# Kernel tuning notes

Measured on AMD Instinct MI355X. Metric: run time of the kernel, lower is better.

## Reference

```python
import jax, jax.numpy as jnp
import numpy as np


def setup_inputs() -> dict:
    key = jax.random.key(0)
    ks = jax.random.split(key, 7)
    T, B, D, H, Q = 256, 128, 1024, 2048, 1024
    return {
        "x": jax.random.normal(ks[0], (T, B, D), dtype=jnp.float32),
        "h0": jax.random.normal(ks[1], (B, H), dtype=jnp.float32) * 0.01,
        "W_xh": jax.random.normal(ks[2], (D, H), dtype=jnp.float32) * 0.01,
        "W_hh": jax.random.normal(ks[3], (H, H), dtype=jnp.float32) * 0.01,
        "b_h": jnp.zeros((H,), dtype=jnp.float32),
        "W_hq": jax.random.normal(ks[4], (H, Q), dtype=jnp.float32) * 0.01,
        "b_q": jnp.zeros((Q,), dtype=jnp.float32),
    }


def reference(x, h0, W_xh, W_hh, b_h, W_hq, b_q):
    # x: (T, B, D); vanilla RNN recurrence with ReLU, per-step output projection.
    def step(h, xt):
        h = jax.nn.relu(xt @ W_xh + h @ W_hh + b_h)  # (B, H)
        return h, h @ W_hq + b_q                      # (B, Q)

    h, outs = jax.lax.scan(step, h0, x)               # outs: (T, B, Q)
    out = outs.reshape(-1, outs.shape[-1])            # torch.cat along dim 0 -> (T*B, Q)
    return out, h
```

## Files before the change

kernel.cpp:

```cpp
#include <hip/hip_runtime.h>
#include <hip/hip_bf16.h>

typedef __bf16 bf16_t;
typedef bf16_t bf16x8 __attribute__((ext_vector_type(8)));
typedef bf16_t bf16x4 __attribute__((ext_vector_type(4)));
typedef bf16_t bf16x2 __attribute__((ext_vector_type(2)));
typedef float f32x4 __attribute__((ext_vector_type(4)));
typedef float f32x2 __attribute__((ext_vector_type(2)));

__device__ __forceinline__ void load_lds16(const bf16_t* g, bf16_t* l) {
  __builtin_amdgcn_global_load_lds(
      (const __attribute__((address_space(1))) unsigned int*)g,
      (__attribute__((address_space(3))) unsigned int*)l,
      16, 0, 0);
}

__global__ void conv_f32_bf16(const float* __restrict__ src,
                              bf16_t* __restrict__ dst, long n) {
  long i = ((long)blockIdx.x * blockDim.x + threadIdx.x) * 8;
  if (i + 7 >= n) return;
  float4 a = *(const float4*)(src + i);
  float4 b = *(const float4*)(src + i + 4);
  bf16x8 v;
  v[0] = (bf16_t)a.x; v[1] = (bf16_t)a.y; v[2] = (bf16_t)a.z; v[3] = (bf16_t)a.w;
  v[4] = (bf16_t)b.x; v[5] = (bf16_t)b.y; v[6] = (bf16_t)b.z; v[7] = (bf16_t)b.w;
  *(bf16x8*)(dst + i) = v;
}

__global__ void conv_bf16_f32(const bf16_t* __restrict__ src,
                              float* __restrict__ dst, long n) {
  long i = (long)blockIdx.x * blockDim.x + threadIdx.x;
  if (i >= n) return;
  dst[i] = (float)src[i];
}

__global__ void transpose_conv(const float* __restrict__ src,
                               bf16_t* __restrict__ dst, int Ksrc, int Nsrc) {
  __shared__ float tile[32][33];
  int n0 = blockIdx.x * 32, k0 = blockIdx.y * 32;
  int tx = threadIdx.x, ty = threadIdx.y;
#pragma unroll
  for (int i = 0; i < 32; i += 8)
    tile[ty + i][tx] = src[(long)(k0 + ty + i) * Nsrc + n0 + tx];
  __syncthreads();
#pragma unroll
  for (int i = 0; i < 32; i += 8)
    dst[(long)(n0 + ty + i) * Ksrc + k0 + tx] = (bf16_t)tile[tx][ty + i];
}

template <int STORE_MODE>
__global__ __launch_bounds__(256) void gemm_bt_128(
    const bf16_t* __restrict__ A, const bf16_t* __restrict__ Bt,
    const float* __restrict__ bias, void* __restrict__ Dout,
    int M, int N, int K) {
  __shared__ bf16_t As[128 * 32];
  __shared__ bf16_t Bs[128 * 32];
  const int tid = threadIdx.x;
  const int lane = tid & 63;
  const int w = tid >> 6;
  const int wr = w >> 1, wc = w & 1;
  const int m0 = blockIdx.y * 128, n0 = blockIdx.x * 128;

  f32x4 acc[4][4] = {};

  const int r0 = tid >> 2;
  const int kk = (tid & 3) * 8;
  const int fr = lane & 15;
  const int fk = (lane >> 4) * 8;

  for (int k0 = 0; k0 < K; k0 += 32) {
    load_lds16(A + (long)(m0 + r0) * K + k0 + kk, As + w * 512);
    load_lds16(A + (long)(m0 + 64 + r0) * K + k0 + kk, As + 2048 + w * 512);
    load_lds16(Bt + (long)(n0 + r0) * K + k0 + kk, Bs + w * 512);
    load_lds16(Bt + (long)(n0 + 64 + r0) * K + k0 + kk, Bs + 2048 + w * 512);
    asm volatile("s_waitcnt vmcnt(0)" ::: "memory");
    __syncthreads();

    bf16x8 af[4], bfx[4];
#pragma unroll
    for (int m = 0; m < 4; ++m)
      af[m] = *(const bf16x8*)&As[(wr * 64 + m * 16 + fr) * 32 + fk];
#pragma unroll
    for (int n = 0; n < 4; ++n)
      bfx[n] = *(const bf16x8*)&Bs[(wc * 64 + n * 16 + fr) * 32 + fk];
#pragma unroll
    for (int m = 0; m < 4; ++m)
#pragma unroll
      for (int n = 0; n < 4; ++n)
        acc[m][n] = __builtin_amdgcn_mfma_f32_16x16x32_bf16(af[m], bfx[n],
                                                            acc[m][n], 0, 0, 0);
    __syncthreads();
  }

  const int fq = lane >> 4;
#pragma unroll
  for (int m = 0; m < 4; ++m) {
#pragma unroll
    for (int n = 0; n < 4; ++n) {
      int col = n0 + wc * 64 + n * 16 + fr;
      float bv = bias[col];
#pragma unroll
      for (int r = 0; r < 4; ++r) {
        int row = m0 + wr * 64 + m * 16 + fq * 4 + r;
        float v = acc[m][n][r] + bv;
        if (STORE_MODE == 0)
          ((float*)Dout)[(long)row * N + col] = v;
        else
          ((bf16_t*)Dout)[(long)row * N + col] = (bf16_t)v;
      }
    }
  }
}

__device__ __forceinline__ void half_bar(unsigned int* c, unsigned int target,
                                         int lane) {
  if (lane == 0)
    __hip_atomic_fetch_add(c, 1u, __ATOMIC_RELEASE,
                           __HIP_MEMORY_SCOPE_WORKGROUP);
  unsigned int v;
  do {
    v = __hip_atomic_load(c, __ATOMIC_ACQUIRE, __HIP_MEMORY_SCOPE_WORKGROUP);
    if (v >= target) break;
    __builtin_amdgcn_s_sleep(1);
  } while (true);
}

__global__ __launch_bounds__(512, 1) void rnn_persistent10(
    const bf16_t* __restrict__ h0,
    bf16_t* __restrict__ Hbuf,
    const bf16_t* __restrict__ WhhT,
    unsigned int* __restrict__ flags) {
  __shared__ bf16_t Wlds[65536];
  __shared__ float sred[2][4][16 * 36];
  __shared__ unsigned int barc[2];
  __shared__ unsigned int sfree[2];

  const int tid = threadIdx.x, lane = tid & 63, w = tid >> 6;
  const int h = w >> 2;
  const int lw = w & 3;
  const int gid = blockIdx.x;
  const int p = (gid >> 1) & 3;
  const int n0idx = ((gid & 1) << 5) | (gid >> 3);
  const int chain = p + h * 4;
  const int m0 = chain * 16, n0 = n0idx * 32;
  const int H = 2048;
  const long BH = 128L * 2048;
  const int kb = lw * 512;
  const int fr = lane & 15, fg = lane >> 4;
  const int w64 = lw * 64;

  {
    const int scol = tid >> 4;
    const int sk16 = tid & 15;
    const bf16_t* gsrc = WhhT + (long)(n0 + scol) * H + sk16 * 8;
#pragma unroll 4
    for (int j = 0; j < 16; ++j) {
      bf16x8 v = *(const bf16x8*)(gsrc + j * 128);
      int k8 = sk16 + j * 16;
      *(bf16x8*)&Wlds[(k8 * 32 + scol) * 8] = v;
    }
  }
  if (tid < 2) { barc[tid] = 0; sfree[tid] = 0; }
  __syncthreads();

  if (h == 1) __builtin_amdgcn_s_sleep(64);

  const int zrowW = lane >> 2, zcolW = (lane & 3) * 8;
  const int sidx = zrowW * 36 + zcolW;
  const long zoffW = (long)(m0 + zrowW) * H + n0 + zcolW;

  unsigned int* myflag = flags + (((chain << 6) | n0idx) << 4);
  const unsigned int* pollflag =
      flags + (((chain << 6) | (lw * 16 + (lane & 15))) << 4);
  unsigned int* bc = &barc[h];
  unsigned int* sf = &sfree[h];

  for (int t = 0; t < 256; ++t) {
    const bf16_t* hp = (t == 0) ? h0 : Hbuf + (long)(t - 1) * BH;
    bf16_t* z = Hbuf + (long)t * BH;

    f32x4 zvr;
    if (lw == 0) {
      const bf16_t* zp = z + zoffW;
      asm volatile("global_load_dwordx4 %0, %1, off sc0 sc1"
                   : "=v"(zvr)
                   : "v"(zp)
                   : "memory");
    }

    if (t > 0) {
      const unsigned int tt = (unsigned int)t;
      unsigned int v = __hip_atomic_load(pollflag, __ATOMIC_RELAXED,
                                         __HIP_MEMORY_SCOPE_AGENT);
      if (!__all(v >= tt)) {
        __builtin_amdgcn_s_sleep(2);
        v = __hip_atomic_load(pollflag, __ATOMIC_RELAXED,
                              __HIP_MEMORY_SCOPE_AGENT);
        if (!__all(v >= tt)) {
          __builtin_amdgcn_s_sleep(4);
          v = __hip_atomic_load(pollflag, __ATOMIC_RELAXED,
                                __HIP_MEMORY_SCOPE_AGENT);
          if (!__all(v >= tt)) {
            __builtin_amdgcn_s_sleep(8);
            v = __hip_atomic_load(pollflag, __ATOMIC_RELAXED,
                                  __HIP_MEMORY_SCOPE_AGENT);
            while (!__all(v >= tt)) {
              __builtin_amdgcn_s_sleep(16);
              v = __hip_atomic_load(pollflag, __ATOMIC_RELAXED,
                                    __HIP_MEMORY_SCOPE_AGENT);
            }
          }
        }
      }
    }

    const bf16_t* Ab = hp + (long)(m0 + fr) * H + kb + fg * 8;
    f32x4 a0, a1, a2, a3, a4, a5, a6, a7, a8, a9, a10, a11, a12, a13, a14, a15;
    asm volatile(
        "global_load_dwordx4 %0, %16, off sc0\n\t"
        "global_load_dwordx4 %1, %16, off offset:64 sc0\n\t"
        "global_load_dwordx4 %2, %16, off offset:128 sc0\n\t"
        "global_load_dwordx4 %3, %16, off offset:192 sc0\n\t"
        "global_load_dwordx4 %4, %16, off offset:256 sc0\n\t"
        "global_load_dwordx4 %5, %16, off offset:320 sc0\n\t"
        "global_load_dwordx4 %6, %16, off offset:384 sc0\n\t"
        "global_load_dwordx4 %7, %16, off offset:448 sc0\n\t"
        "global_load_dwordx4 %8, %16, off offset:512 sc0\n\t"
        "global_load_dwordx4 %9, %16, off offset:576 sc0\n\t"
        "global_load_dwordx4 %10, %16, off offset:640 sc0\n\t"
        "global_load_dwordx4 %11, %16, off offset:704 sc0\n\t"
        "global_load_dwordx4 %12, %16, off offset:768 sc0\n\t"
        "global_load_dwordx4 %13, %16, off offset:832 sc0\n\t"
        "global_load_dwordx4 %14, %16, off offset:896 sc0\n\t"
        "global_load_dwordx4 %15, %16, off offset:960 sc0\n\t"
        "s_waitcnt vmcnt(0)"
        : "=&v"(a0), "=&v"(a1), "=&v"(a2), "=&v"(a3), "=&v"(a4), "=&v"(a5),
          "=&v"(a6), "=&v"(a7), "=&v"(a8), "=&v"(a9), "=&v"(a10), "=&v"(a11),
          "=&v"(a12), "=&v"(a13), "=&v"(a14), "=&v"(a15)
        : "v"(Ab)
        : "memory");
    __builtin_amdgcn_sched_barrier(0);

    f32x4 acc0 = {}, acc1 = {};
#define STEPX(ks, A)                                                          \
  {                                                                           \
    bf16x8 w0 = *(const bf16x8*)&Wlds[((w64 + (ks) * 4 + fg) * 32 + fr) * 8]; \
    bf16x8 w1 =                                                               \
        *(const bf16x8*)&Wlds[((w64 + (ks) * 4 + fg) * 32 + 16 + fr) * 8];    \
    bf16x8 av = __builtin_bit_cast(bf16x8, A);                                \
    acc0 = __builtin_amdgcn_mfma_f32_16x16x32_bf16(av, w0, acc0, 0, 0, 0);    \
    acc1 = __builtin_amdgcn_mfma_f32_16x16x32_bf16(av, w1, acc1, 0, 0, 0);    \
  }
    STEPX(0, a0)   STEPX(1, a1)   STEPX(2, a2)   STEPX(3, a3)
    STEPX(4, a4)   STEPX(5, a5)   STEPX(6, a6)   STEPX(7, a7)
    STEPX(8, a8)   STEPX(9, a9)   STEPX(10, a10) STEPX(11, a11)
    STEPX(12, a12) STEPX(13, a13) STEPX(14, a14) STEPX(15, a15)
#undef STEPX

    if (t > 0) {
      while (__hip_atomic_load(sf, __ATOMIC_ACQUIRE,
                               __HIP_MEMORY_SCOPE_WORKGROUP) <
             (unsigned int)t)
        __builtin_amdgcn_s_sleep(1);
    }

#pragma unroll
    for (int rr = 0; rr < 4; ++rr) {
      sred[h][lw][(fg * 4 + rr) * 36 + fr] = acc0[rr];
      sred[h][lw][(fg * 4 + rr) * 36 + 16 + fr] = acc1[rr];
    }
    half_bar(bc, (unsigned int)(t + 1) * 4, lane);

    if (lw == 0) {
      f32x4 slo = *(const f32x4*)&sred[h][0][sidx];
      f32x4 shi = *(const f32x4*)&sred[h][0][sidx + 4];
#pragma unroll
      for (int ww = 1; ww < 4; ++ww) {
        slo = slo + *(const f32x4*)&sred[h][ww][sidx];
        shi = shi + *(const f32x4*)&sred[h][ww][sidx + 4];
      }
      bf16x8 zv = __builtin_bit_cast(bf16x8, zvr);
      bf16x8 o;
#pragma unroll
      for (int c = 0; c < 4; ++c) {
        float v0 = slo[c] + (float)zv[c];
        float v1 = shi[c] + (float)zv[c + 4];
        o[c] = (bf16_t)(v0 > 0.f ? v0 : 0.f);
        o[c + 4] = (bf16_t)(v1 > 0.f ? v1 : 0.f);
      }
      const bf16_t* zp = z + zoffW;
      {
        f32x4 ov = __builtin_bit_cast(f32x4, o);
        asm volatile("global_store_dwordx4 %0, %1, off sc0 sc1" ::"v"(zp),
                     "v"(ov)
                     : "memory");
      }
      asm volatile("s_waitcnt vmcnt(0)" ::: "memory");
      if (lane == 0) {
        __hip_atomic_store(myflag, (unsigned int)(t + 1), __ATOMIC_RELAXED,
                           __HIP_MEMORY_SCOPE_AGENT);
        __hip_atomic_store(sf, (unsigned int)(t + 1), __ATOMIC_RELEASE,
                           __HIP_MEMORY_SCOPE_WORKGROUP);
      }
    }
  }
}

extern "C" void kernel_launch(void* const* d_in, const int* in_sizes, int n_in,
                              void* d_out, int out_size, void* d_ws,
                              size_t ws_size, hipStream_t stream) {
  const float* x   = (const float*)d_in[0];
  const float* h0  = (const float*)d_in[1];
  const float* Wxh = (const float*)d_in[2];
  const float* Whh = (const float*)d_in[3];
  const float* bh  = (const float*)d_in[4];
  const float* Whq = (const float*)d_in[5];
  const float* bq  = (const float*)d_in[6];
  float* out = (float*)d_out;

  const int T = 256, B = 128, D = 1024, H = 2048, Q = 1024;
  const long MB = (long)T * B;

  char* ws = (char*)d_ws;
  unsigned int* flags = (unsigned int*)ws;  ws += 512 * 64;
  bf16_t* x_bf = (bf16_t*)ws;  ws += MB * D * 2;
  bf16_t* Hbuf = (bf16_t*)ws;  ws += MB * H * 2;
  bf16_t* h0bf = (bf16_t*)ws;  ws += (long)B * H * 2;
  bf16_t* WxhT = (bf16_t*)ws;  ws += (long)H * D * 2;
  bf16_t* WhhT = (bf16_t*)ws;  ws += (long)H * H * 2;
  bf16_t* WhqT = (bf16_t*)ws;  ws += (long)Q * H * 2;

  hipMemsetAsync(flags, 0, 512 * 64, stream);

  conv_f32_bf16<<<(int)(MB * D / 8 / 256), 256, 0, stream>>>(x, x_bf, MB * D);
  conv_f32_bf16<<<(int)((long)B * H / 8 / 256), 256, 0, stream>>>(h0, h0bf,
                                                                  (long)B * H);
  transpose_conv<<<dim3(H / 32, D / 32), dim3(32, 8), 0, stream>>>(Wxh, WxhT, D, H);
  transpose_conv<<<dim3(H / 32, H / 32), dim3(32, 8), 0, stream>>>(Whh, WhhT, H, H);
  transpose_conv<<<dim3(Q / 32, H / 32), dim3(32, 8), 0, stream>>>(Whq, WhqT, H, Q);

  gemm_bt_128<1><<<dim3(H / 128, MB / 128), 256, 0, stream>>>(
      x_bf, WxhT, bh, Hbuf, (int)MB, H, D);

  rnn_persistent10<<<256, 512, 0, stream>>>(h0bf, Hbuf, WhhT, flags);

  gemm_bt_128<0><<<dim3(Q / 128, MB / 128), 256, 0, stream>>>(
      Hbuf, WhqT, bq, out, (int)MB, Q, H);

  conv_bf16_f32<<<(int)((long)B * H / 256), 256, 0, stream>>>(
      Hbuf + (long)(T - 1) * B * H, out + MB * Q, (long)B * H);
}
```

Baseline: 1.762 ms.

## Pack flags contiguously, poll with shorter backoff, split A-load wait across MFMAs

Inter-block flags move from one-per-64-byte slot to densely packed words, so a wave's 16 poll lanes read one contiguous region. Polling now uses an explicit coherent (sc0 sc1) load with a shorter sleep backoff, and the flag store is an explicit sc0 sc1 store. The single wait for all 16 operand loads is split into vmcnt(8) and vmcnt(0), so the first half of the MFMAs can start while the second half of the loads is still in flight. The risks are false sharing on the packed flags and extra polling traffic.

```diff
diff --git a/kernel.cpp b/kernel.cpp
--- a/kernel.cpp
+++ b/kernel.cpp
@@ -125,7 +125,7 @@
   } while (true);
 }
 
-__global__ __launch_bounds__(512, 1) void rnn_persistent10(
+__global__ __launch_bounds__(512, 1) void rnn_persistent12(
     const bf16_t* __restrict__ h0,
     bf16_t* __restrict__ Hbuf,
     const bf16_t* __restrict__ WhhT,
@@ -169,9 +169,8 @@
   const int sidx = zrowW * 36 + zcolW;
   const long zoffW = (long)(m0 + zrowW) * H + n0 + zcolW;
 
-  unsigned int* myflag = flags + (((chain << 6) | n0idx) << 4);
-  const unsigned int* pollflag =
-      flags + (((chain << 6) | (lw * 16 + (lane & 15))) << 4);
+  unsigned int* myflag = flags + ((chain << 6) | n0idx);
+  const unsigned int* pollp = flags + ((chain << 6) | (lw * 16) | (lane & 15));
   unsigned int* bc = &barc[h];
   unsigned int* sf = &sfree[h];
 
@@ -190,28 +189,24 @@
 
     if (t > 0) {
       const unsigned int tt = (unsigned int)t;
-      unsigned int v = __hip_atomic_load(pollflag, __ATOMIC_RELAXED,
-                                         __HIP_MEMORY_SCOPE_AGENT);
+      unsigned int v;
+#define PFLAG                                                                 \
+  asm volatile("global_load_dword %0, %1, off sc0 sc1\n\ts_waitcnt vmcnt(0)"  \
+               : "=v"(v) : "v"(pollp) : "memory");
+      PFLAG
       if (!__all(v >= tt)) {
-        __builtin_amdgcn_s_sleep(2);
-        v = __hip_atomic_load(pollflag, __ATOMIC_RELAXED,
-                              __HIP_MEMORY_SCOPE_AGENT);
+        __builtin_amdgcn_s_sleep(1);
+        PFLAG
         if (!__all(v >= tt)) {
-          __builtin_amdgcn_s_sleep(4);
-          v = __hip_atomic_load(pollflag, __ATOMIC_RELAXED,
-                                __HIP_MEMORY_SCOPE_AGENT);
-          if (!__all(v >= tt)) {
-            __builtin_amdgcn_s_sleep(8);
-            v = __hip_atomic_load(pollflag, __ATOMIC_RELAXED,
-                                  __HIP_MEMORY_SCOPE_AGENT);
-            while (!__all(v >= tt)) {
-              __builtin_amdgcn_s_sleep(16);
-              v = __hip_atomic_load(pollflag, __ATOMIC_RELAXED,
-                                    __HIP_MEMORY_SCOPE_AGENT);
-            }
+          __builtin_amdgcn_s_sleep(2);
+          PFLAG
+          while (!__all(v >= tt)) {
+            __builtin_amdgcn_s_sleep(4);
+            PFLAG
           }
         }
       }
+#undef PFLAG
     }
 
     const bf16_t* Ab = hp + (long)(m0 + fr) * H + kb + fg * 8;
@@ -232,14 +227,12 @@
         "global_load_dwordx4 %12, %16, off offset:768 sc0\n\t"
         "global_load_dwordx4 %13, %16, off offset:832 sc0\n\t"
         "global_load_dwordx4 %14, %16, off offset:896 sc0\n\t"
-        "global_load_dwordx4 %15, %16, off offset:960 sc0\n\t"
-        "s_waitcnt vmcnt(0)"
+        "global_load_dwordx4 %15, %16, off offset:960 sc0"
         : "=&v"(a0), "=&v"(a1), "=&v"(a2), "=&v"(a3), "=&v"(a4), "=&v"(a5),
           "=&v"(a6), "=&v"(a7), "=&v"(a8), "=&v"(a9), "=&v"(a10), "=&v"(a11),
           "=&v"(a12), "=&v"(a13), "=&v"(a14), "=&v"(a15)
         : "v"(Ab)
         : "memory");
-    __builtin_amdgcn_sched_barrier(0);
 
     f32x4 acc0 = {}, acc1 = {};
 #define STEPX(ks, A)                                                          \
@@ -251,8 +244,12 @@
     acc0 = __builtin_amdgcn_mfma_f32_16x16x32_bf16(av, w0, acc0, 0, 0, 0);    \
     acc1 = __builtin_amdgcn_mfma_f32_16x16x32_bf16(av, w1, acc1, 0, 0, 0);    \
   }
+    asm volatile("s_waitcnt vmcnt(8)" ::: "memory");
+    __builtin_amdgcn_sched_barrier(0);
     STEPX(0, a0)   STEPX(1, a1)   STEPX(2, a2)   STEPX(3, a3)
     STEPX(4, a4)   STEPX(5, a5)   STEPX(6, a6)   STEPX(7, a7)
+    asm volatile("s_waitcnt vmcnt(0)" ::: "memory");
+    __builtin_amdgcn_sched_barrier(0);
     STEPX(8, a8)   STEPX(9, a9)   STEPX(10, a10) STEPX(11, a11)
     STEPX(12, a12) STEPX(13, a13) STEPX(14, a14) STEPX(15, a15)
 #undef STEPX
@@ -297,9 +294,11 @@
       }
       asm volatile("s_waitcnt vmcnt(0)" ::: "memory");
       if (lane == 0) {
-        __hip_atomic_store(myflag, (unsigned int)(t + 1), __ATOMIC_RELAXED,
-                           __HIP_MEMORY_SCOPE_AGENT);
-        __hip_atomic_store(sf, (unsigned int)(t + 1), __ATOMIC_RELEASE,
+        unsigned int fv = (unsigned int)(t + 1);
+        asm volatile("global_store_dword %0, %1, off sc0 sc1" ::"v"(myflag),
+                     "v"(fv)
+                     : "memory");
+        __hip_atomic_store(sf, fv, __ATOMIC_RELEASE,
                            __HIP_MEMORY_SCOPE_WORKGROUP);
       }
     }
@@ -342,7 +341,7 @@
   gemm_bt_128<1><<<dim3(H / 128, MB / 128), 256, 0, stream>>>(
       x_bf, WxhT, bh, Hbuf, (int)MB, H, D);
 
-  rnn_persistent10<<<256, 512, 0, stream>>>(h0bf, Hbuf, WhhT, flags);
+  rnn_persistent12<<<256, 512, 0, stream>>>(h0bf, Hbuf, WhhT, flags);
 
   gemm_bt_128<0><<<dim3(Q / 128, MB / 128), 256, 0, stream>>>(
       Hbuf, WhqT, bq, out, (int)MB, Q, H);
```

After: 3.660 ms. +107.7%, slower.
